# Kernel tuning notes

Measured on AMD Instinct MI355X. Metric: run time of the kernel, lower is better.

## Reference

```python
import jax, jax.numpy as jnp
import numpy as np

N_STATE = 1024
N_HEAD = 16
B, S = 2, 2048
NEG = -1e9  # finite stand-in for -inf in the additive causal mask


def setup_inputs() -> dict:
    key = jax.random.key(0)
    ks = jax.random.split(key, 8)
    sd = N_STATE ** -0.5
    x = jax.random.normal(ks[0], (B, S, N_STATE), dtype=jnp.float32)
    # additive causal mask, as in Whisper: upper triangle = -inf
    i = jnp.arange(S)
    mask = jnp.where(i[None, :] > i[:, None], NEG, 0.0).astype(jnp.float32)
    return {
        "x": x,
        "mask": mask,
        "Wq": jax.random.normal(ks[1], (N_STATE, N_STATE), jnp.float32) * sd,
        "bq": jax.random.normal(ks[2], (N_STATE,), jnp.float32) * 0.02,
        "Wk": jax.random.normal(ks[3], (N_STATE, N_STATE), jnp.float32) * sd,
        "Wv": jax.random.normal(ks[4], (N_STATE, N_STATE), jnp.float32) * sd,
        "bv": jax.random.normal(ks[5], (N_STATE,), jnp.float32) * 0.02,
        "Wo": jax.random.normal(ks[6], (N_STATE, N_STATE), jnp.float32) * sd,
        "bo": jax.random.normal(ks[7], (N_STATE,), jnp.float32) * 0.02,
    }


def reference(x, mask, Wq, bq, Wk, Wv, bv, Wo, bo):
    B_, S_, D = x.shape
    H = N_HEAD
    hd = D // H
    scale = hd ** -0.25  # applied to both q and k, per the source

    q = (x @ Wq + bq).reshape(B_, S_, H, hd) * scale   # [B,S,H,hd]
    k = (x @ Wk).reshape(B_, S_, H, hd) * scale        # key has no bias
    v = (x @ Wv + bv).reshape(B_, S_, H, hd)

    qk = jnp.einsum("bqhd,bkhd->bhqk", q, k) + mask[:S_, :S_]
    w = jax.nn.softmax(qk.astype(jnp.float32), axis=-1).astype(q.dtype)
    o = jnp.einsum("bhqk,bkhd->bqhd", w, v).reshape(B_, S_, D)
    return o @ Wo + bo
```

## Files before the change

### kernel.cpp

```cpp
#include <hip/hip_runtime.h>
#include <hip/hip_bf16.h>

#define BB 2
#define SS 2048
#define DD 1024
#define HH 16
#define HD 64
#define QKSCALE 0.35355339059327373f
#define QKSCALE_E2 0.42466090144f
#define NEGBIG (-1e9f)

using u16 = unsigned short;
typedef __attribute__((ext_vector_type(8))) short short8;
typedef __attribute__((ext_vector_type(4))) float floatx4;
typedef __attribute__((ext_vector_type(4))) unsigned short ushort4v;

#define GLOBAL_AS __attribute__((address_space(1)))
#define LDS_AS __attribute__((address_space(3)))

__device__ __forceinline__ u16 f2b(float f) {
  union { float f; unsigned u; } v; v.f = f;
  return (u16)((v.u + 0x7fffu + ((v.u >> 16) & 1u)) >> 16);
}

__device__ __forceinline__ u16 bconv(float f) {
  union { __hip_bfloat16 h; u16 u; } cv;
  cv.h = __float2bfloat16(f);
  return cv.u;
}

__device__ __forceinline__ float ex2(float f) {
  return __builtin_amdgcn_exp2f(f);
}

__device__ __forceinline__ floatx4 vmax4(floatx4 a, floatx4 b) {
  return (floatx4){fmaxf(a[0], b[0]), fmaxf(a[1], b[1]),
                   fmaxf(a[2], b[2]), fmaxf(a[3], b[3])};
}

__device__ __forceinline__ void gload_lds16(const void* g, void* l) {
  __builtin_amdgcn_global_load_lds((GLOBAL_AS void*)(g), (LDS_AS void*)(l), 16, 0, 0);
}

__global__ __launch_bounds__(256) void cvt_bf16x4(const float4* __restrict__ src,
                                                  ushort4v* __restrict__ dst, int n4) {
  int i = blockIdx.x * 256 + threadIdx.x;
  if (i >= n4) return;
  float4 f = src[i];
  ushort4v o = { f2b(f.x), f2b(f.y), f2b(f.z), f2b(f.w) };
  dst[i] = o;
}

__global__ __launch_bounds__(256) void transpose_w(const float* __restrict__ s0,
                                                   const float* __restrict__ s1,
                                                   const float* __restrict__ s2,
                                                   const float* __restrict__ s3,
                                                   u16* __restrict__ dst) {
  __shared__ float tile[32][33];
  const float* src = (blockIdx.z == 0) ? s0 : (blockIdx.z == 1) ? s1
                   : (blockIdx.z == 2) ? s2 : s3;
  u16* d = dst + (size_t)blockIdx.z * 1024 * 1024;
  int c0 = blockIdx.x * 32, r0 = blockIdx.y * 32;
  int tx = threadIdx.x, ty = threadIdx.y;
#pragma unroll
  for (int i = 0; i < 4; ++i)
    tile[ty + i * 8][tx] = src[(size_t)(r0 + ty + i * 8) * 1024 + c0 + tx];
  __syncthreads();
#pragma unroll
  for (int i = 0; i < 4; ++i)
    d[(size_t)(c0 + ty + i * 8) * 1024 + r0 + tx] = f2b(tile[tx][ty + i * 8]);
}

__global__ __launch_bounds__(256) void transpose_v(const u16* __restrict__ v,
                                                   u16* __restrict__ vtd) {
  __shared__ u16 tile[32][34];
  int b = blockIdx.z;
  int c0 = blockIdx.x * 32;
  int s0 = blockIdx.y * 32;
  int tx = threadIdx.x, ty = threadIdx.y;
#pragma unroll
  for (int i = 0; i < 4; ++i)
    tile[ty + i * 8][tx] = v[(size_t)(b * SS + s0 + ty + i * 8) * DD + c0 + tx];
  __syncthreads();
#pragma unroll
  for (int i = 0; i < 4; ++i)
    vtd[(size_t)(b * DD + c0 + ty + i * 8) * SS + s0 + tx] = tile[tx][ty + i * 8];
}

template <typename OutT>
__global__ __launch_bounds__(256, 3)
void gemm_bt(const u16* __restrict__ A, const u16* __restrict__ Bt,
             OutT* __restrict__ C, const float* __restrict__ bias,
             float scale, int M, int N, int K) {
  const int tid = threadIdx.x;
  const int lane = tid & 63;
  const int w = tid >> 6;
  const int id = (int)blockIdx.x;
  const int swz = (id & 7) * 64 + (id >> 3);
  const int m0 = (swz & 63) * 64;
  const int n0 = (swz >> 6) * 128;
  __shared__ u16 As[2][64 * 64];
  __shared__ u16 Bs[2][128 * 64];
  floatx4 acc[2][4];
#pragma unroll
  for (int i = 0; i < 2; ++i)
#pragma unroll
    for (int j = 0; j < 4; ++j) acc[i][j] = (floatx4){0.f, 0.f, 0.f, 0.f};

  const int wr = (w >> 1) * 32;
  const int wc = (w & 1) * 64;
  const int g = lane >> 4;
  const int lr = lane & 15;
  const size_t strideA = (size_t)K * 2;

  auto stage = [&](int k0, int buf) {
#pragma unroll
    for (int p = 0; p < 2; ++p) {
      int L = tid * 16 + p * 4096;
      int row = L >> 7;
      int cb = (L ^ ((row & 7) << 4)) & 127;
      gload_lds16((const char*)A + (size_t)(m0 + row) * strideA + k0 * 2 + cb,
                  (char*)As[buf] + p * 4096 + w * 1024);
    }
#pragma unroll
    for (int p = 0; p < 4; ++p) {
      int L = tid * 16 + p * 4096;
      int row = L >> 7;
      int cb = (L ^ ((row & 7) << 4)) & 127;
      gload_lds16((const char*)Bt + (size_t)(n0 + row) * strideA + k0 * 2 + cb,
                  (char*)Bs[buf] + p * 4096 + w * 1024);
    }
  };

  const int nsteps = K >> 6;
  stage(0, 0);
  for (int t = 0; t < nsteps; ++t) {
    const int buf = t & 1;
    __syncthreads();
    if (t + 1 < nsteps) stage((t + 1) << 6, buf ^ 1);
    const u16* as = As[buf];
    const u16* bs = Bs[buf];
#pragma unroll
    for (int ks = 0; ks < 2; ++ks) {
      short8 af[2], bf[4];
      const int c0 = ks * 32 + g * 8;
#pragma unroll
      for (int mi = 0; mi < 2; ++mi) {
        int row = wr + mi * 16 + lr;
        af[mi] = *(const short8*)(as + row * 64 + (c0 ^ ((row & 7) << 3)));
      }
#pragma unroll
      for (int ni = 0; ni < 4; ++ni) {
        int row = wc + ni * 16 + lr;
        bf[ni] = *(const short8*)(bs + row * 64 + (c0 ^ ((row & 7) << 3)));
      }
      __builtin_amdgcn_s_setprio(1);
#pragma unroll
      for (int mi = 0; mi < 2; ++mi)
#pragma unroll
        for (int ni = 0; ni < 4; ++ni)
          acc[mi][ni] = __builtin_amdgcn_mfma_f32_16x16x32_bf16(af[mi], bf[ni],
                                                                acc[mi][ni], 0, 0, 0);
      __builtin_amdgcn_s_setprio(0);
    }
  }
#pragma unroll
  for (int ni = 0; ni < 4; ++ni) {
    int col = n0 + wc + ni * 16 + lr;
    float bvv = bias ? bias[col] : 0.f;
#pragma unroll
    for (int mi = 0; mi < 2; ++mi) {
#pragma unroll
      for (int r = 0; r < 4; ++r) {
        int rowg = m0 + wr + mi * 16 + g * 4 + r;
        float val = (acc[mi][ni][r] + bvv) * scale;
        if constexpr (sizeof(OutT) == 4) C[(size_t)rowg * N + col] = val;
        else C[(size_t)rowg * N + col] = (OutT)f2b(val);
      }
    }
  }
}

__global__ __launch_bounds__(256, 4)
void gemm_qkv(const u16* __restrict__ A, const u16* __restrict__ Wt3,
              u16* __restrict__ Out3, const float* __restrict__ bq,
              const float* __restrict__ bv) {
  const int id = (int)blockIdx.x;
  const int swz = (id & 7) * 96 + (id >> 3);
  const int bx = swz & 31;
  const int rest = swz >> 5;
  const int by = rest & 7;
  const int seg = rest >> 3;
  const u16* Bt = Wt3 + (size_t)seg * 1024 * 1024;
  u16* C = Out3 + (size_t)seg * 4096 * 1024;
  const float* bias = (seg == 0) ? bq : (seg == 2) ? bv : nullptr;
  const float scale = (seg == 2) ? 1.0f : QKSCALE_E2;

  const int tid = threadIdx.x;
  const int lane = tid & 63;
  const int w = tid >> 6;
  const int m0 = bx * 128;
  const int n0 = by * 128;
  __shared__ u16 As[2][64 * 64];
  __shared__ u16 Bs[2][64 * 64];
  floatx4 acc[4][4];
#pragma unroll
  for (int i = 0; i < 4; ++i)
#pragma unroll
    for (int j = 0; j < 4; ++j) acc[i][j] = (floatx4){0.f, 0.f, 0.f, 0.f};
  const int wr = (w >> 1) * 64;
  const int wc = (w & 1) * 64;
  const int g = lane >> 4;
  const int lr = lane & 15;

  auto stage = [&](int k0, int buf) {
#pragma unroll
    for (int p = 0; p < 2; ++p) {
      int L = tid * 16 + p * 4096;
      int lrow = L >> 7;
      int un = (L & 127) ^ ((lrow & 7) << 4);
      int r = lrow * 2 + (un >> 6);
      int cb = un & 63;
      gload_lds16((const char*)A + (size_t)(m0 + r) * 2048 + k0 * 2 + cb,
                  (char*)As[buf] + p * 4096 + w * 1024);
      gload_lds16((const char*)Bt + (size_t)(n0 + r) * 2048 + k0 * 2 + cb,
                  (char*)Bs[buf] + p * 4096 + w * 1024);
    }
  };

  stage(0, 0);
  for (int t = 0; t < 32; ++t) {
    const int buf = t & 1;
    __syncthreads();
    if (t + 1 < 32) stage((t + 1) << 5, buf ^ 1);
    const u16* as = As[buf];
    const u16* bs = Bs[buf];
    short8 af[4], bf[4];
#pragma unroll
    for (int mi = 0; mi < 4; ++mi) {
      int r = wr + mi * 16 + lr;
      af[mi] = *(const short8*)((const char*)as +
               ((r >> 1) * 128 + ((((r & 1) << 6) | (g * 16)) ^ (((r >> 1) & 7) << 4))));
    }
#pragma unroll
    for (int ni = 0; ni < 4; ++ni) {
      int r = wc + ni * 16 + lr;
      bf[ni] = *(const short8*)((const char*)bs +
               ((r >> 1) * 128 + ((((r & 1) << 6) | (g * 16)) ^ (((r >> 1) & 7) << 4))));
    }
    __builtin_amdgcn_s_setprio(1);
#pragma unroll
    for (int mi = 0; mi < 4; ++mi)
#pragma unroll
      for (int ni = 0; ni < 4; ++ni)
        acc[mi][ni] = __builtin_amdgcn_mfma_f32_16x16x32_bf16(af[mi], bf[ni],
                                                              acc[mi][ni], 0, 0, 0);
    __builtin_amdgcn_s_setprio(0);
  }

  __syncthreads();
  u16* eb = (w == 0) ? (u16*)As[0] : (w == 1) ? (u16*)As[1]
          : (w == 2) ? (u16*)Bs[0] : (u16*)Bs[1];
  const int rr = lane >> 2;
  const int cc = lane & 3;
  float bv4[4];
#pragma unroll
  for (int ni = 0; ni < 4; ++ni)
    bv4[ni] = bias ? bias[n0 + wc + ni * 16 + lr] : 0.f;
#pragma unroll
  for (int mi = 0; mi < 4; ++mi) {
#pragma unroll
    for (int ni = 0; ni < 4; ++ni)
#pragma unroll
      for (int r = 0; r < 4; ++r)
        eb[(g * 4 + r) * 72 + ni * 16 + lr] =
            f2b((acc[mi][ni][r] + bv4[ni]) * scale);
    short8 v0 = *(const short8*)(eb + rr * 72 + cc * 16);
    short8 v1 = *(const short8*)(eb + rr * 72 + cc * 16 + 8);
    u16* dst = C + (size_t)(m0 + wr + mi * 16 + rr) * 1024 + n0 + wc + cc * 16;
    *(short8*)dst = v0;
    *(short8*)(dst + 8) = v1;
  }
}

__device__ __forceinline__ void stream_softmax(floatx4 (&sa)[4], float& m, float& l,
                                               floatx4 (&acc)[4], u16* pl,
                                               bool diag, int wlr, int g, int lr) {
  if (diag) {
#pragma unroll
    for (int ct = 0; ct < 4; ++ct)
#pragma unroll
      for (int r = 0; r < 4; ++r)
        if (ct * 16 + g * 4 + r > wlr) sa[ct][r] += NEGBIG;
  }
  floatx4 v = vmax4(vmax4(sa[0], sa[1]), vmax4(sa[2], sa[3]));
  float mx = fmaxf(fmaxf(v[0], v[1]), fmaxf(v[2], v[3]));
  mx = fmaxf(mx, __shfl_xor(mx, 16, 64));
  mx = fmaxf(mx, __shfl_xor(mx, 32, 64));
  if (!__all(mx <= m + 8.f)) {
    float mn = fmaxf(m, mx);
    float al = ex2(m - mn);
    l *= al;
#pragma unroll
    for (int dt = 0; dt < 4; ++dt) acc[dt] *= al;
    m = mn;
  }
  floatx4 p[4];
#pragma unroll
  for (int ct = 0; ct < 4; ++ct)
#pragma unroll
    for (int r = 0; r < 4; ++r)
      p[ct][r] = ex2(sa[ct][r] - m);
  floatx4 s = (p[0] + p[1]) + (p[2] + p[3]);
  float rs = (s[0] + s[1]) + (s[2] + s[3]);
  rs += __shfl_xor(rs, 16, 64);
  rs += __shfl_xor(rs, 32, 64);
  l += rs;
#pragma unroll
  for (int ct = 0; ct < 4; ++ct) {
    ushort4v pk = { bconv(p[ct][0]), bconv(p[ct][1]),
                    bconv(p[ct][2]), bconv(p[ct][3]) };
    *(ushort4v*)((char*)pl + ((lr * 128 + ct * 32 + g * 8) ^ ((lr & 7) << 4))) = pk;
  }
}

__global__ __launch_bounds__(256, 4)
void flash_attn(const u16* __restrict__ q, const u16* __restrict__ k,
                const u16* __restrict__ vt, u16* __restrict__ o) {
  const int tid = threadIdx.x;
  const int lane = tid & 63;
  const int w = tid >> 6;
  const int g = lane >> 4;
  const int lr = lane & 15;
  const int i = (int)blockIdx.x;
  const int x = i & 7;
  const int kk = i >> 3;
  const int s = kk & 3;
  const int mI = kk >> 2;
  const int u = mI >> 3;
  const int v = mI & 7;
  const int gg = x * 4 + s;
  const int b = gg >> 4;
  const int h = gg & 15;
  const int a = (u + s) & 3;
  const int qt = (a == 0) ? v : (a == 1) ? (31 - v) : (a == 2) ? (16 + v) : (15 - v);
  const int row0 = qt * 64 + w * 16;
  const int wlr = w * 16 + lr;

  __shared__ u16 Ks[2][64 * 64];
  __shared__ u16 Vs[2][64 * 64];
  __shared__ u16 Pl[4][16 * 64];

  short8 qf[2];
  {
    const u16* qp = q + (size_t)(b * SS + row0 + lr) * DD + h * HD + g * 8;
    qf[0] = *(const short8*)qp;
    qf[1] = *(const short8*)(qp + 32);
  }
  floatx4 acc[4];
#pragma unroll
  for (int dt = 0; dt < 4; ++dt) acc[dt] = (floatx4){0.f, 0.f, 0.f, 0.f};
  float m = -1e30f, l = 0.f;

  const char* kbase = (const char*)(k + (size_t)(b * SS) * DD + h * HD);
  const char* vbase = (const char*)(vt + (size_t)((b * HH + h) * HD) * SS);
  const int nt = qt + 1;

  auto stage = [&](int t, int buf) {
    const int kvb = t * 64;
#pragma unroll
    for (int p = 0; p < 2; ++p) {
      int L = tid * 16 + p * 4096;
      int row = L >> 7;
      int cb = (L ^ ((row & 7) << 4)) & 127;
      gload_lds16(kbase + (size_t)(kvb + row) * (DD * 2) + cb,
                  (char*)Ks + buf * 8192 + p * 4096 + w * 1024);
      gload_lds16(vbase + (size_t)row * (SS * 2) + kvb * 2 + cb,
                  (char*)Vs + buf * 8192 + p * 4096 + w * 1024);
    }
  };

  stage(0, 0);
  int cur = 0;
  for (int t = 0; t < nt; ++t) {
    __syncthreads();
    if (t + 1 < nt) stage(t + 1, cur ^ 1);
    const u16* kc = Ks[cur];
    const u16* vc = Vs[cur];

    floatx4 sa[4];
#pragma unroll
    for (int ct = 0; ct < 4; ++ct) sa[ct] = (floatx4){0.f, 0.f, 0.f, 0.f};
    __builtin_amdgcn_s_setprio(1);
#pragma unroll
    for (int ks = 0; ks < 2; ++ks) {
      const int c0 = ks * 32 + g * 8;
#pragma unroll
      for (int ct = 0; ct < 4; ++ct) {
        int row = ct * 16 + lr;
        short8 kf = *(const short8*)(kc + row * 64 + (c0 ^ ((row & 7) << 3)));
        sa[ct] = __builtin_amdgcn_mfma_f32_16x16x32_bf16(kf, qf[ks], sa[ct], 0, 0, 0);
      }
    }
    __builtin_amdgcn_s_setprio(0);

    stream_softmax(sa, m, l, acc, Pl[w], t == qt, wlr, g, lr);

    __builtin_amdgcn_s_setprio(1);
#pragma unroll
    for (int ks = 0; ks < 2; ++ks) {
      const int c0 = ks * 32 + g * 8;
      int pby = (lr * 128 + ks * 64 + g * 16) ^ ((lr & 7) << 4);
      short8 pf = *(const short8*)((const char*)Pl[w] + pby);
#pragma unroll
      for (int dt = 0; dt < 4; ++dt) {
        int row = dt * 16 + lr;
        short8 vf = *(const short8*)(vc + row * 64 + (c0 ^ ((row & 7) << 3)));
        acc[dt] = __builtin_amdgcn_mfma_f32_16x16x32_bf16(vf, pf, acc[dt], 0, 0, 0);
      }
    }
    __builtin_amdgcn_s_setprio(0);
    cur ^= 1;
  }

  float inv = 1.0f / l;
#pragma unroll
  for (int dt = 0; dt < 4; ++dt) {
    ushort4v pa = { bconv(acc[dt][0] * inv), bconv(acc[dt][1] * inv),
                    bconv(acc[dt][2] * inv), bconv(acc[dt][3] * inv) };
    *(ushort4v*)(o + (size_t)(b * SS + row0 + lr) * DD + h * HD + dt * 16 + g * 4) = pa;
  }
}

extern "C" void kernel_launch(void* const* d_in, const int* in_sizes, int n_in,
                              void* d_out, int out_size, void* d_ws, size_t ws_size,
                              hipStream_t stream) {
  const float* x  = (const float*)d_in[0];
  const float* Wq = (const float*)d_in[2];
  const float* bq = (const float*)d_in[3];
  const float* Wk = (const float*)d_in[4];
  const float* Wv = (const float*)d_in[5];
  const float* bv = (const float*)d_in[6];
  const float* Wo = (const float*)d_in[7];
  const float* bo = (const float*)d_in[8];
  float* out = (float*)d_out;

  char* ws = (char*)d_ws;
  u16* xb  = (u16*)(ws);
  u16* wt  = (u16*)(ws + (8u << 20));
  u16* qkv = (u16*)(ws + (16u << 20));
  u16* vb  = qkv + 2u * 4096 * 1024;
  u16* vtb = (u16*)(ws + (40u << 20));
  u16* ob  = (u16*)(ws + (48u << 20));
  u16* wot = wt + 3u * 1024 * 1024;

  dim3 tb(32, 8);
  cvt_bf16x4<<<4096, 256, 0, stream>>>((const float4*)x, (ushort4v*)xb,
                                       (BB * SS * DD) / 4);
  transpose_w<<<dim3(32, 32, 4), tb, 0, stream>>>(Wq, Wk, Wv, Wo, wt);
  gemm_qkv<<<768, 256, 0, stream>>>(xb, wt, qkv, bq, bv);
  transpose_v<<<dim3(32, 64, 2), tb, 0, stream>>>(vb, vtb);
  flash_attn<<<1024, 256, 0, stream>>>(qkv, qkv + (size_t)4096 * 1024, vtb, ob);
  gemm_bt<float><<<512, 256, 0, stream>>>(ob, wot, out, bo, 1.0f,
                                          4096, 1024, 1024);
}
```

Measured before the change: 113.5 us.

## Restructure flash attention into single-wave blocks with direct global K/V loads

Each attention block becomes one 64-lane wavefront handling 32 query rows (two 16-row groups) instead of four waves sharing 64 rows. K and V fragments are now read straight from global memory into registers, replacing the LDS double buffer and the block-wide barriers. The causal work is balanced by pairing short and long row tiles through the index mapping. This removes synchronisation and LDS staging, but each wave now loads K/V separately, so global and L2 traffic rises and there is no explicit prefetch to hide load latency.

```diff
diff --git a/kernel.cpp b/kernel.cpp
--- a/kernel.cpp
+++ b/kernel.cpp
@@ -285,13 +285,13 @@
 
 __device__ __forceinline__ void stream_softmax(floatx4 (&sa)[4], float& m, float& l,
                                                floatx4 (&acc)[4], u16* pl,
-                                               bool diag, int wlr, int g, int lr) {
+                                               bool diag, int wl, int g, int lr) {
   if (diag) {
 #pragma unroll
     for (int ct = 0; ct < 4; ++ct)
 #pragma unroll
       for (int r = 0; r < 4; ++r)
-        if (ct * 16 + g * 4 + r > wlr) sa[ct][r] += NEGBIG;
+        if (ct * 16 + g * 4 + r > wl) sa[ct][r] += NEGBIG;
   }
   floatx4 v = vmax4(vmax4(sa[0], sa[1]), vmax4(sa[2], sa[3]));
   float mx = fmaxf(fmaxf(v[0], v[1]), fmaxf(v[2], v[3]));
@@ -324,111 +324,115 @@
   }
 }
 
-__global__ __launch_bounds__(256, 4)
+__global__ __launch_bounds__(64)
 void flash_attn(const u16* __restrict__ q, const u16* __restrict__ k,
                 const u16* __restrict__ vt, u16* __restrict__ o) {
-  const int tid = threadIdx.x;
-  const int lane = tid & 63;
-  const int w = tid >> 6;
+  const int lane = threadIdx.x;
   const int g = lane >> 4;
   const int lr = lane & 15;
   const int i = (int)blockIdx.x;
   const int x = i & 7;
-  const int kk = i >> 3;
-  const int s = kk & 3;
-  const int mI = kk >> 2;
-  const int u = mI >> 3;
-  const int v = mI & 7;
-  const int gg = x * 4 + s;
-  const int b = gg >> 4;
-  const int h = gg & 15;
-  const int a = (u + s) & 3;
-  const int qt = (a == 0) ? v : (a == 1) ? (31 - v) : (a == 2) ? (16 + v) : (15 - v);
-  const int row0 = qt * 64 + w * 16;
-  const int wlr = w * 16 + lr;
-
-  __shared__ u16 Ks[2][64 * 64];
-  __shared__ u16 Vs[2][64 * 64];
-  __shared__ u16 Pl[4][16 * 64];
-
-  short8 qf[2];
+  const int rest = i >> 3;
+  const int head = x * 4 + (rest >> 6);
+  const int idx = rest & 63;
+  const int b = head >> 4;
+  const int h = head & 15;
+  const int j = (idx & 1) ? (idx >> 1) : (63 - (idx >> 1));
+  const int R = j * 32;
+  const int nt = ((R + 31) >> 6) + 1;
+  const int dT = nt - 1;
+  const int RA = R, RB = R + 16;
+  const int wlA = (RA & 63);
+  const int wlB = (RB & 63);
+
+  __shared__ u16 Pl[2][16 * 64];
+
+  short8 qfA[2], qfB[2];
   {
-    const u16* qp = q + (size_t)(b * SS + row0 + lr) * DD + h * HD + g * 8;
-    qf[0] = *(const short8*)qp;
-    qf[1] = *(const short8*)(qp + 32);
-  }
-  floatx4 acc[4];
-#pragma unroll
-  for (int dt = 0; dt < 4; ++dt) acc[dt] = (floatx4){0.f, 0.f, 0.f, 0.f};
-  float m = -1e30f, l = 0.f;
+    const u16* qa = q + (size_t)(b * SS + RA + lr) * DD + h * HD + g * 8;
+    qfA[0] = *(const short8*)qa;
+    qfA[1] = *(const short8*)(qa + 32);
+    const u16* qb = q + (size_t)(b * SS + RB + lr) * DD + h * HD + g * 8;
+    qfB[0] = *(const short8*)qb;
+    qfB[1] = *(const short8*)(qb + 32);
+  }
+  floatx4 accA[4], accB[4];
+#pragma unroll
+  for (int dt = 0; dt < 4; ++dt) {
+    accA[dt] = (floatx4){0.f, 0.f, 0.f, 0.f};
+    accB[dt] = (floatx4){0.f, 0.f, 0.f, 0.f};
+  }
+  float mA = -1e30f, lA = 0.f, mB = -1e30f, lB = 0.f;
 
   const char* kbase = (const char*)(k + (size_t)(b * SS) * DD + h * HD);
   const char* vbase = (const char*)(vt + (size_t)((b * HH + h) * HD) * SS);
-  const int nt = qt + 1;
-
-  auto stage = [&](int t, int buf) {
+
+  for (int t = 0; t < nt; ++t) {
     const int kvb = t * 64;
-#pragma unroll
-    for (int p = 0; p < 2; ++p) {
-      int L = tid * 16 + p * 4096;
-      int row = L >> 7;
-      int cb = (L ^ ((row & 7) << 4)) & 127;
-      gload_lds16(kbase + (size_t)(kvb + row) * (DD * 2) + cb,
-                  (char*)Ks + buf * 8192 + p * 4096 + w * 1024);
-      gload_lds16(vbase + (size_t)row * (SS * 2) + kvb * 2 + cb,
-                  (char*)Vs + buf * 8192 + p * 4096 + w * 1024);
-    }
-  };
-
-  stage(0, 0);
-  int cur = 0;
-  for (int t = 0; t < nt; ++t) {
-    __syncthreads();
-    if (t + 1 < nt) stage(t + 1, cur ^ 1);
-    const u16* kc = Ks[cur];
-    const u16* vc = Vs[cur];
-
-    floatx4 sa[4];
-#pragma unroll
-    for (int ct = 0; ct < 4; ++ct) sa[ct] = (floatx4){0.f, 0.f, 0.f, 0.f};
+    short8 kf[8];
+#pragma unroll
+    for (int ks = 0; ks < 2; ++ks)
+#pragma unroll
+      for (int ct = 0; ct < 4; ++ct)
+        kf[ks * 4 + ct] = *(const short8*)(kbase +
+            (size_t)(kvb + ct * 16 + lr) * (DD * 2) + (ks * 32 + g * 8) * 2);
+
+    floatx4 saA[4], saB[4];
+#pragma unroll
+    for (int ct = 0; ct < 4; ++ct) {
+      saA[ct] = (floatx4){0.f, 0.f, 0.f, 0.f};
+      saB[ct] = (floatx4){0.f, 0.f, 0.f, 0.f};
+    }
     __builtin_amdgcn_s_setprio(1);
 #pragma unroll
+    for (int ks = 0; ks < 2; ++ks)
+#pragma unroll
+      for (int ct = 0; ct < 4; ++ct) {
+        saA[ct] = __builtin_amdgcn_mfma_f32_16x16x32_bf16(kf[ks * 4 + ct], qfA[ks],
+                                                          saA[ct], 0, 0, 0);
+        saB[ct] = __builtin_amdgcn_mfma_f32_16x16x32_bf16(kf[ks * 4 + ct], qfB[ks],
+                                                          saB[ct], 0, 0, 0);
+      }
+    __builtin_amdgcn_s_setprio(0);
+
+    short8 vf[8];
+#pragma unroll
+    for (int ks = 0; ks < 2; ++ks)
+#pragma unroll
+      for (int dt = 0; dt < 4; ++dt)
+        vf[ks * 4 + dt] = *(const short8*)(vbase +
+            (size_t)(dt * 16 + lr) * (SS * 2) + (kvb + ks * 32 + g * 8) * 2);
+
+    stream_softmax(saA, mA, lA, accA, Pl[0], t == dT, wlA + lr, g, lr);
+    stream_softmax(saB, mB, lB, accB, Pl[1], t == dT, wlB + lr, g, lr);
+
+    __builtin_amdgcn_s_setprio(1);
+#pragma unroll
     for (int ks = 0; ks < 2; ++ks) {
-      const int c0 = ks * 32 + g * 8;
-#pragma unroll
-      for (int ct = 0; ct < 4; ++ct) {
-        int row = ct * 16 + lr;
-        short8 kf = *(const short8*)(kc + row * 64 + (c0 ^ ((row & 7) << 3)));
-        sa[ct] = __builtin_amdgcn_mfma_f32_16x16x32_bf16(kf, qf[ks], sa[ct], 0, 0, 0);
+      int pby = (lr * 128 + ks * 64 + g * 16) ^ ((lr & 7) << 4);
+      short8 pfA = *(const short8*)((const char*)Pl[0] + pby);
+      short8 pfB = *(const short8*)((const char*)Pl[1] + pby);
+#pragma unroll
+      for (int dt = 0; dt < 4; ++dt) {
+        accA[dt] = __builtin_amdgcn_mfma_f32_16x16x32_bf16(vf[ks * 4 + dt], pfA,
+                                                           accA[dt], 0, 0, 0);
+        accB[dt] = __builtin_amdgcn_mfma_f32_16x16x32_bf16(vf[ks * 4 + dt], pfB,
+                                                           accB[dt], 0, 0, 0);
       }
     }
     __builtin_amdgcn_s_setprio(0);
-
-    stream_softmax(sa, m, l, acc, Pl[w], t == qt, wlr, g, lr);
-
-    __builtin_amdgcn_s_setprio(1);
-#pragma unroll
-    for (int ks = 0; ks < 2; ++ks) {
-      const int c0 = ks * 32 + g * 8;
-      int pby = (lr * 128 + ks * 64 + g * 16) ^ ((lr & 7) << 4);
-      short8 pf = *(const short8*)((const char*)Pl[w] + pby);
-#pragma unroll
-      for (int dt = 0; dt < 4; ++dt) {
-        int row = dt * 16 + lr;
-        short8 vf = *(const short8*)(vc + row * 64 + (c0 ^ ((row & 7) << 3)));
-        acc[dt] = __builtin_amdgcn_mfma_f32_16x16x32_bf16(vf, pf, acc[dt], 0, 0, 0);
-      }
-    }
-    __builtin_amdgcn_s_setprio(0);
-    cur ^= 1;
-  }
-
-  float inv = 1.0f / l;
+  }
+
+  float invA = 1.0f / lA;
+  float invB = 1.0f / lB;
 #pragma unroll
   for (int dt = 0; dt < 4; ++dt) {
-    ushort4v pa = { bconv(acc[dt][0] * inv), bconv(acc[dt][1] * inv),
-                    bconv(acc[dt][2] * inv), bconv(acc[dt][3] * inv) };
-    *(ushort4v*)(o + (size_t)(b * SS + row0 + lr) * DD + h * HD + dt * 16 + g * 4) = pa;
+    ushort4v pa = { bconv(accA[dt][0] * invA), bconv(accA[dt][1] * invA),
+                    bconv(accA[dt][2] * invA), bconv(accA[dt][3] * invA) };
+    ushort4v pb = { bconv(accB[dt][0] * invB), bconv(accB[dt][1] * invB),
+                    bconv(accB[dt][2] * invB), bconv(accB[dt][3] * invB) };
+    *(ushort4v*)(o + (size_t)(b * SS + RA + lr) * DD + h * HD + dt * 16 + g * 4) = pa;
+    *(ushort4v*)(o + (size_t)(b * SS + RB + lr) * DD + h * HD + dt * 16 + g * 4) = pb;
   }
 }
 
@@ -460,7 +464,7 @@
   transpose_w<<<dim3(32, 32, 4), tb, 0, stream>>>(Wq, Wk, Wv, Wo, wt);
   gemm_qkv<<<768, 256, 0, stream>>>(xb, wt, qkv, bq, bv);
   transpose_v<<<dim3(32, 64, 2), tb, 0, stream>>>(vb, vtb);
-  flash_attn<<<1024, 256, 0, stream>>>(qkv, qkv + (size_t)4096 * 1024, vtb, ob);
+  flash_attn<<<2048, 64, 0, stream>>>(qkv, qkv + (size_t)4096 * 1024, vtb, ob);
   gemm_bt<float><<<512, 256, 0, stream>>>(ob, wot, out, bo, 1.0f,
                                           4096, 1024, 1024);
 }
```

New measurement: 174.5 us. 53.8% more time.
